# Kernel optimization log

Hardware: AMD Instinct MI355X
Metric: run time of the kernel (lower is better)

Reference implementation:

```python
import jax, jax.numpy as jnp
import numpy as np

B, V, T = 1, 1, 2
C = 128          # in_features
H = 4            # num_heads
NKV = 12288      # cells at cross zoom 5 (12*4**5)
S = NKV          # query groups == cross cells
NH = 9           # neighborhood size (cell + 8 ring)
NPQ = 16         # queries per group: 4**(7-5)
NQ = S * NPQ     # cells at zoom 7


def _ln(x, scale, bias, eps=1e-5):
    mu = jnp.mean(x, axis=-1, keepdims=True)
    var = jnp.mean(jnp.square(x - mu), axis=-1, keepdims=True)
    return (x - mu) * jax.lax.rsqrt(var + eps) * scale + bias


def setup_inputs() -> dict:
    key = jax.random.key(0)
    ks = jax.random.split(key, 12)
    w = lambda k, shp: jax.random.normal(k, shp, jnp.float32) * (1.0 / np.sqrt(shp[0]))
    return {
        "x_q":  jax.random.normal(ks[0], (B, V, T, NQ, C), jnp.float32),
        "x_kv": jax.random.normal(ks[1], (B, V, T, NKV, C), jnp.float32),
        "nh_idx":  jax.random.randint(ks[2], (S, NH), 0, NKV, jnp.int32),
        "nh_mask": jnp.ones((S, NH), jnp.bool_),
        "ln_q_s": jnp.ones((C,), jnp.float32), "ln_q_b": jnp.zeros((C,), jnp.float32),
        "Wq": w(ks[3], (C, C)), "bq": jnp.zeros((C,), jnp.float32),
        "ln_kv_s": jnp.ones((C,), jnp.float32), "ln_kv_b": jnp.zeros((C,), jnp.float32),
        "Wkv": w(ks[4], (C, 2 * C)), "bkv": jnp.zeros((2 * C,), jnp.float32),
        "Wa_q": w(ks[5], (C, C)),
        "W_out": w(ks[6], (C, C)), "b_out": jnp.zeros((C,), jnp.float32),
        "gamma": jnp.full((C,), 1e-6, jnp.float32),
        "ln_m_s": jnp.ones((C,), jnp.float32), "ln_m_b": jnp.zeros((C,), jnp.float32),
        "Wm": w(ks[7], (C, C)), "bm": jnp.zeros((C,), jnp.float32),
        "W1": w(ks[8], (C, C)), "b1": jnp.zeros((C,), jnp.float32),
        "W2": w(ks[9], (C, C)), "b2": jnp.zeros((C,), jnp.float32),
        "gamma_mlp": jnp.full((C,), 1e-6, jnp.float32),
    }


def reference(x_q, x_kv, nh_idx, nh_mask, ln_q_s, ln_q_b, Wq, bq,
              ln_kv_s, ln_kv_b, Wkv, bkv, Wa_q, W_out, b_out, gamma,
              ln_m_s, ln_m_b, Wm, bm, W1, b1, W2, b2, gamma_mlp):
    hd = C // H
    # q_layer: LN + Linear
    q = _ln(x_q, ln_q_s, ln_q_b) @ Wq + bq                      # [B,V,T,NQ,C]
    # kv_layer: LN + Linear to 2C (K|V)
    kv = _ln(x_kv, ln_kv_s, ln_kv_b) @ Wkv + bkv                # [B,V,T,NKV,2C]
    # grid neighborhood gather (get_nh)
    kv_nh = kv[:, :, :, nh_idx, :]                              # [B,V,T,S,NH,2C]
    k, vv = jnp.split(kv_nh, 2, axis=-1)                        # [B,V,T,S,NH,C] each
    # group queries per cross cell
    q = q.reshape(B, V, T, S, NPQ, C)
    # cross attention (q projected inside attention; k/v pre-projected)
    qh = (q @ Wa_q).reshape(B, V, T, S, NPQ, H, hd)
    kh = k.reshape(B, V, T, S, NH, H, hd)
    vh = vv.reshape(B, V, T, S, NH, H, hd)
    scores = jnp.einsum('bvtsqhd,bvtsnhd->bvtshqn', qh, kh) / np.sqrt(hd)
    bias = jnp.where(nh_mask, 0.0, -1e9).astype(scores.dtype)   # mask==False -> masked
    scores = scores + bias[None, None, None, :, None, None, :]
    attn = jax.nn.softmax(scores, axis=-1)
    out = jnp.einsum('bvtshqn,bvtsnhd->bvtsqhd', attn, vh).reshape(B, V, T, S, NPQ, C)
    out = out @ W_out + b_out
    x = x_q + gamma * out.reshape(B, V, T, NQ, C)
    # gated MLP residual
    h = _ln(x, ln_m_s, ln_m_b) @ Wm + bm
    m = jax.nn.gelu(h @ W1 + b1) @ W2 + b2
    x = x + gamma_mlp * m
    return x
```

## Files before the change

### kernel.cpp

```cpp
#include <hip/hip_runtime.h>
#include <hip/hip_bf16.h>

#define DEVINL __device__ __forceinline__

typedef __attribute__((ext_vector_type(8))) short bf16x8;
typedef __attribute__((ext_vector_type(4))) float f32x4;

static constexpr int SS = 12288;
static constexpr float QKS = 0.17677669529663687f;

DEVINL f32x4 f32x4_zero() { f32x4 z; z[0]=0.f; z[1]=0.f; z[2]=0.f; z[3]=0.f; return z; }
DEVINL f32x4 mfma16(bf16x8 a, bf16x8 b, f32x4 c) {
  return __builtin_amdgcn_mfma_f32_16x16x32_bf16(a, b, c, 0, 0, 0);
}
DEVINL unsigned short f2bf(float f) {
  __hip_bfloat16 h = __float2bfloat16(f);
  return __builtin_bit_cast(unsigned short, h);
}
DEVINL float bf2f(unsigned short u) {
  unsigned v = ((unsigned)u) << 16;
  return __builtin_bit_cast(float, v);
}
DEVINL unsigned cvt_pk_bf16(float lo_, float hi_) {
  unsigned r;
  asm volatile("v_cvt_pk_bf16_f32 %0, %1, %2" : "=v"(r) : "v"(lo_), "v"(hi_));
  return r;
}
DEVINL int swz(int r, int c) {
  return (r << 7) + ((((c >> 3) ^ (r & 7))) << 3) + (c & 7);
}
DEVINL void wave_sync() {
  asm volatile("s_waitcnt lgkmcnt(0)" ::: "memory");
  __builtin_amdgcn_sched_barrier(0);
}
DEVINL float gelu_f(float x) {
  float u = 0.7978845608028654f * (x + 0.044715f * x * x * x);
  float t = 1.0f - 2.0f / (__expf(2.0f * u) + 1.0f);
  return 0.5f * x * (1.0f + t);
}

DEVINL void stage8(const unsigned short* __restrict__ wf_all,
                   unsigned short* slot, int slice, int tid) {
  const unsigned short* src = wf_all + (size_t)slice * 4096;
  const int wv = tid >> 6, l = tid & 63;
#pragma unroll
  for (int r = 0; r < 2; ++r) {
    int off = (r * 4 + wv) * 512;
    __builtin_amdgcn_global_load_lds(
        (const __attribute__((address_space(1))) unsigned int*)(src + off + l * 8),
        (__attribute__((address_space(3))) unsigned int*)(slot + off), 16, 0, 0);
  }
}

__global__ void prep_weights(const float* __restrict__ w0, const float* __restrict__ w1,
                             const float* __restrict__ w2, const float* __restrict__ w3,
                             const float* __restrict__ w4, const float* __restrict__ w5,
                             unsigned short* __restrict__ wfrag) {
  int gid = blockIdx.x * 256 + threadIdx.x;
  int i  = gid & 7;
  int l  = (gid >> 3) & 63;
  int mt = (gid >> 9) & 7;
  int kt = (gid >> 12) & 3;
  int mat = gid >> 14;
  const float* W = (mat == 0) ? w0 : (mat == 1) ? w1 : (mat == 2) ? w2
                 : (mat == 3) ? w3 : (mat == 4) ? w4 : w5;
  int k = kt * 32 + (l >> 4) * 8 + i;
  int c = mt * 16 + (l & 15);
  float v = W[k * 128 + c];
  if (mat == 1) v *= QKS;
  wfrag[gid] = f2bf(v);
}

__global__ __launch_bounds__(256) void kv_proj(
    const float* __restrict__ xkv, const float* __restrict__ lns,
    const float* __restrict__ lnb, const float* __restrict__ Wkv,
    const float* __restrict__ bkv, unsigned short* __restrict__ kvout) {
  __shared__ float y[16][132];
  const int tid = threadIdx.x;
  const size_t rb = (size_t)blockIdx.x * 16;
  {
    int r = tid >> 4, p = tid & 15;
    const float* xr = xkv + (rb + r) * 128 + p * 8;
    float v[8];
    float sum = 0.f, sq = 0.f;
#pragma unroll
    for (int i = 0; i < 2; ++i) {
      float4 q4 = *(const float4*)(xr + i * 4);
      v[i*4+0]=q4.x; v[i*4+1]=q4.y; v[i*4+2]=q4.z; v[i*4+3]=q4.w;
      sum += q4.x + q4.y + q4.z + q4.w;
      sq  += q4.x*q4.x + q4.y*q4.y + q4.z*q4.z + q4.w*q4.w;
    }
    sum += __shfl_xor(sum, 1, 16); sum += __shfl_xor(sum, 2, 16);
    sum += __shfl_xor(sum, 4, 16); sum += __shfl_xor(sum, 8, 16);
    sq  += __shfl_xor(sq, 1, 16);  sq  += __shfl_xor(sq, 2, 16);
    sq  += __shfl_xor(sq, 4, 16);  sq  += __shfl_xor(sq, 8, 16);
    float mu = sum * (1.0f/128.f);
    float rs = rsqrtf(sq * (1.0f/128.f) - mu*mu + 1e-5f);
#pragma unroll
    for (int i = 0; i < 8; ++i) {
      int c = p * 8 + i;
      y[r][c] = (v[i] - mu) * rs * lns[c] + lnb[c];
    }
  }
  __syncthreads();
  const int c2 = tid;
  float acc[16];
#pragma unroll
  for (int r = 0; r < 16; ++r) acc[r] = 0.f;
  for (int c = 0; c < 128; c += 4) {
    float w0 = Wkv[(c+0)*256 + c2];
    float w1 = Wkv[(c+1)*256 + c2];
    float w2 = Wkv[(c+2)*256 + c2];
    float w3 = Wkv[(c+3)*256 + c2];
#pragma unroll
    for (int r = 0; r < 16; ++r) {
      float4 yv = *(const float4*)&y[r][c];
      acc[r] += yv.x*w0 + yv.y*w1 + yv.z*w2 + yv.w*w3;
    }
  }
  float bb = bkv[c2];
#pragma unroll
  for (int r = 0; r < 16; ++r)
    kvout[(rb + r) * 256 + c2] = f2bf(acc[r] + bb);
}

template <int MODE>
DEVINL void mmFlip(unsigned short* X, unsigned short (*Wb)[4096],
                   const unsigned short* __restrict__ wf_all, int j0,
                   const float* __restrict__ bias,
                   const float* __restrict__ xqw, const float* __restrict__ gamma,
                   unsigned* x2p, const float* __restrict__ gmlp,
                   float* __restrict__ outw, int tid) {
  const int l = tid & 63, lo = l & 15, g = l >> 4;
  f32x4 acc[8];
#pragma unroll
  for (int mt = 0; mt < 8; ++mt) acc[mt] = f32x4_zero();

#pragma unroll
  for (int kt = 0; kt < 4; ++kt) {
    const int j = j0 + kt;
    if (j + 1 < 24) stage8(wf_all, Wb[(j + 1) & 1], j + 1, tid);
    const unsigned short* W = Wb[j & 1];
    bf16x8 b = *(const bf16x8*)(X + swz(lo, kt * 32 + g * 8));
#pragma unroll
    for (int mt = 0; mt < 8; ++mt) {
      bf16x8 a = *(const bf16x8*)(W + (mt * 64 + l) * 8);
      acc[mt] = mfma16(a, b, acc[mt]);
    }
    __syncthreads();
  }

#pragma unroll
  for (int mt = 0; mt < 8; ++mt) {
    int c0 = mt * 16 + g * 4;
    float v0 = acc[mt][0], v1 = acc[mt][1], v2 = acc[mt][2], v3 = acc[mt][3];
    if (bias) {
      float4 b4 = *(const float4*)(bias + c0);
      v0 += b4.x; v1 += b4.y; v2 += b4.z; v3 += b4.w;
    }
    if (MODE == 1) { v0 = gelu_f(v0); v1 = gelu_f(v1); v2 = gelu_f(v2); v3 = gelu_f(v3); }
    if (MODE == 2) {
      float4 x4 = *(const float4*)(xqw + lo * 128 + c0);
      float4 g4 = *(const float4*)(gamma + c0);
      v0 = x4.x + g4.x * v0; v1 = x4.y + g4.y * v1;
      v2 = x4.z + g4.z * v2; v3 = x4.w + g4.w * v3;
      x2p[2 * mt]     = cvt_pk_bf16(v0, v1);
      x2p[2 * mt + 1] = cvt_pk_bf16(v2, v3);
    } else if (MODE == 3) {
      float4 p4 = *(const float4*)(gmlp + c0);
      unsigned xa = x2p[2 * mt], xb = x2p[2 * mt + 1];
      float4 o;
      o.x = bf2f((unsigned short)(xa & 0xffff))  + p4.x * v0;
      o.y = bf2f((unsigned short)(xa >> 16))     + p4.y * v1;
      o.z = bf2f((unsigned short)(xb & 0xffff))  + p4.z * v2;
      o.w = bf2f((unsigned short)(xb >> 16))     + p4.w * v3;
      *(float4*)(outw + lo * 128 + c0) = o;
    } else {
      uint2 w2;
      w2.x = cvt_pk_bf16(v0, v1);
      w2.y = cvt_pk_bf16(v2, v3);
      *(uint2*)(X + swz(lo, c0)) = w2;
    }
  }
}

__global__ __launch_bounds__(256, 3) void fused_main(
    const float* __restrict__ xq, const int* __restrict__ nh_idx,
    const unsigned char* __restrict__ nh_mask,
    const unsigned short* __restrict__ wfrag,
    const unsigned short* __restrict__ kvws,
    const float* __restrict__ ln_q_s, const float* __restrict__ ln_q_b,
    const float* __restrict__ bq, const float* __restrict__ b_out,
    const float* __restrict__ gamma, const float* __restrict__ ln_m_s,
    const float* __restrict__ ln_m_b, const float* __restrict__ bm,
    const float* __restrict__ b1, const float* __restrict__ b2,
    const float* __restrict__ gmlp, float* __restrict__ out) {
  __shared__ __align__(16) unsigned short Wb[2][4096];
  __shared__ __align__(16) unsigned short SU[4][3200];

  const int tid = threadIdx.x, l = tid & 63, wv = tid >> 6;
  const int lo = l & 15, g = l >> 4;
  const int nwg = gridDim.x;
  const int cpx = nwg >> 3;
  const int bid = (blockIdx.x & 7) * cpx + (blockIdx.x >> 3);
  const int su = bid * 4 + wv;
  const int t = su / SS, s = su - t * SS;
  const float* xqw = xq + (size_t)su * 2048;
  float* outw = out + (size_t)su * 2048;
  unsigned short* X = SU[wv];
  unsigned short* K = SU[wv] + 2048;

  stage8(wfrag, Wb[0], 0, tid);
  float sbias[4];
#pragma unroll
  for (int e = 0; e < 4; ++e) {
    int n = g * 4 + e;
    sbias[e] = (n < 9) ? (nh_mask[s * 9 + n] ? 0.0f : -1e9f) : -1e9f;
  }
  uint4 gr[5];
  {
#pragma unroll
    for (int i = 0; i < 5; ++i) {
      int idx = i * 64 + l;
      if (idx < 288) {
        int n = idx >> 5, ch = idx & 31;
        int jrow = nh_idx[s * 9 + n];
        gr[i] = *(const uint4*)(kvws + ((size_t)(t * SS + jrow)) * 256 + ch * 8);
      }
    }
#pragma unroll
    for (int i = 0; i < 5; ++i) {
      int idx = i * 64 + l;
      if (idx < 288 && (idx & 31) < 16) {
        int n = idx >> 5, ch = idx & 31;
        *(uint4*)(K + n * 128 + ((ch ^ (n & 7)) << 3)) = gr[i];
      }
    }
  }

  {
    float4 xv[8];
    float sum = 0.f, sq = 0.f;
#pragma unroll
    for (int mt = 0; mt < 8; ++mt) {
      xv[mt] = *(const float4*)(xqw + lo * 128 + mt * 16 + g * 4);
      sum += xv[mt].x + xv[mt].y + xv[mt].z + xv[mt].w;
      sq  += xv[mt].x*xv[mt].x + xv[mt].y*xv[mt].y + xv[mt].z*xv[mt].z + xv[mt].w*xv[mt].w;
    }
    sum += __shfl_xor(sum, 16); sum += __shfl_xor(sum, 32);
    sq  += __shfl_xor(sq, 16);  sq  += __shfl_xor(sq, 32);
    float mu = sum * (1.0f/128.f);
    float rs = rsqrtf(sq * (1.0f/128.f) - mu*mu + 1e-5f);
#pragma unroll
    for (int mt = 0; mt < 8; ++mt) {
      int c0 = mt * 16 + g * 4;
      float4 s4 = *(const float4*)(ln_q_s + c0);
      float4 b4 = *(const float4*)(ln_q_b + c0);
      uint2 w2;
      w2.x = cvt_pk_bf16((xv[mt].x - mu) * rs * s4.x + b4.x,
                         (xv[mt].y - mu) * rs * s4.y + b4.y);
      w2.y = cvt_pk_bf16((xv[mt].z - mu) * rs * s4.z + b4.z,
                         (xv[mt].w - mu) * rs * s4.w + b4.w);
      *(uint2*)(X + swz(lo, c0)) = w2;
    }
  }
  wave_sync();
  __syncthreads();

  unsigned x2p[16];

  mmFlip<0>(X, Wb, wfrag, 0, bq, nullptr, nullptr, nullptr, nullptr, nullptr, tid);
  wave_sync();
  mmFlip<0>(X, Wb, wfrag, 4, nullptr, nullptr, nullptr, nullptr, nullptr, nullptr, tid);
  wave_sync();

  {
    const int krow = (lo > 8) ? 8 : lo;
    f32x4 st[4];
    __builtin_amdgcn_s_setprio(1);
#pragma unroll
    for (int h = 0; h < 4; ++h) {
      bf16x8 ka = *(const bf16x8*)(K + swz(krow, h * 32 + g * 8));
      bf16x8 qb = *(const bf16x8*)(X + swz(lo,   h * 32 + g * 8));
      st[h] = mfma16(ka, qb, f32x4_zero());
    }
    __builtin_amdgcn_s_setprio(0);
    wave_sync();
#pragma unroll
    for (int i = 0; i < 5; ++i) {
      int idx = i * 64 + l;
      if (idx < 288 && (idx & 31) >= 16) {
        int n = idx >> 5, d0 = ((idx & 31) - 16) * 8;
        int nt = d0 >> 4;
        int base = nt * 256 + (n >> 1) * 32 + (d0 & 15) * 2 + (n & 1);
        const unsigned short* u = (const unsigned short*)&gr[i];
#pragma unroll
        for (int dd = 0; dd < 8; ++dd) X[base + dd * 2] = u[dd];
      }
    }
    bf16x8 pfrag[4];
#pragma unroll
    for (int h = 0; h < 4; ++h) {
      float p0 = st[h][0] + sbias[0], p1 = st[h][1] + sbias[1];
      float p2 = st[h][2] + sbias[2], p3 = st[h][3] + sbias[3];
      float m = fmaxf(fmaxf(p0, p1), fmaxf(p2, p3));
      m = fmaxf(m, __shfl_xor(m, 16)); m = fmaxf(m, __shfl_xor(m, 32));
      p0 = __expf(p0 - m); p1 = __expf(p1 - m);
      p2 = __expf(p2 - m); p3 = __expf(p3 - m);
      float ss = p0 + p1 + p2 + p3;
      ss += __shfl_xor(ss, 16); ss += __shfl_xor(ss, 32);
      float inv = 1.0f / ss;
      p0 *= inv; p1 *= inv; p2 *= inv; p3 *= inv;
      float b0 = __shfl_xor(p0, 16), b1 = __shfl_xor(p1, 16),
            b2_ = __shfl_xor(p2, 16), b3 = __shfl_xor(p3, 16);
      float c0_ = __shfl_xor(p0, 32), c1 = __shfl_xor(p1, 32),
            c2 = __shfl_xor(p2, 32), c3 = __shfl_xor(p3, 32);
      float d0_ = __shfl_xor(p0, 48), d1 = __shfl_xor(p1, 48),
            d2 = __shfl_xor(p2, 48), d3 = __shfl_xor(p3, 48);
      float L0 = (g == 0) ? p0 : (g == 1) ? d0_ : 0.f;
      float L1 = (g == 0) ? p1 : (g == 1) ? d1 : 0.f;
      float L2 = (g == 0) ? p2 : (g == 1) ? d2 : 0.f;
      float L3 = (g == 0) ? p3 : (g == 1) ? d3 : 0.f;
      float H0 = (g == 0) ? b0 : (g == 1) ? c0_ : 0.f;
      float H1 = (g == 0) ? b1 : (g == 1) ? c1 : 0.f;
      float H2 = (g == 0) ? b2_ : (g == 1) ? c2 : 0.f;
      float H3 = (g == 0) ? b3 : (g == 1) ? c3 : 0.f;
      uint4 pu;
      pu.x = cvt_pk_bf16(L0, L1); pu.y = cvt_pk_bf16(L2, L3);
      pu.z = cvt_pk_bf16(H0, H1); pu.w = cvt_pk_bf16(H2, H3);
      pfrag[h] = __builtin_bit_cast(bf16x8, pu);
    }
    wave_sync();
    f32x4 oacc[8];
    __builtin_amdgcn_s_setprio(1);
#pragma unroll
    for (int nt = 0; nt < 8; ++nt) {
      unsigned vw0 = 0, vw1 = 0, vw2 = 0, vw3 = 0;
      if (g < 2) {
        const unsigned short* vb = X + nt * 256 + g * 128 + lo * 2;
        vw0 = *(const unsigned*)(vb);
        vw1 = *(const unsigned*)(vb + 32);
        vw2 = *(const unsigned*)(vb + 64);
        vw3 = *(const unsigned*)(vb + 96);
      }
      uint4 vu; vu.x = vw0; vu.y = vw1; vu.z = vw2; vu.w = vw3;
      bf16x8 vfrag = __builtin_bit_cast(bf16x8, vu);
      oacc[nt] = mfma16(pfrag[nt >> 1], vfrag, f32x4_zero());
    }
    __builtin_amdgcn_s_setprio(0);
    wave_sync();
#pragma unroll
    for (int nt = 0; nt < 8; ++nt)
#pragma unroll
      for (int e = 0; e < 4; ++e)
        X[swz(g * 4 + e, nt * 16 + lo)] = (unsigned short)(cvt_pk_bf16(oacc[nt][e], 0.f) & 0xffff);
    wave_sync();
  }

  mmFlip<2>(X, Wb, wfrag, 8, b_out, xqw, gamma, x2p, nullptr, nullptr, tid);

  {
    float sum = 0.f, sq = 0.f;
#pragma unroll
    for (int mt = 0; mt < 8; ++mt) {
      unsigned xa = x2p[2*mt], xb = x2p[2*mt+1];
      float v0 = bf2f((unsigned short)(xa & 0xffff));
      float v1 = bf2f((unsigned short)(xa >> 16));
      float v2 = bf2f((unsigned short)(xb & 0xffff));
      float v3 = bf2f((unsigned short)(xb >> 16));
      sum += v0 + v1 + v2 + v3;
      sq  += v0*v0 + v1*v1 + v2*v2 + v3*v3;
    }
    sum += __shfl_xor(sum, 16); sum += __shfl_xor(sum, 32);
    sq  += __shfl_xor(sq, 16);  sq  += __shfl_xor(sq, 32);
    float mu = sum * (1.0f/128.f);
    float rs = rsqrtf(sq * (1.0f/128.f) - mu*mu + 1e-5f);
#pragma unroll
    for (int mt = 0; mt < 8; ++mt) {
      int c0 = mt * 16 + g * 4;
      unsigned xa = x2p[2*mt], xb = x2p[2*mt+1];
      float4 s4 = *(const float4*)(ln_m_s + c0);
      float4 b4 = *(const float4*)(ln_m_b + c0);
      uint2 w2;
      w2.x = cvt_pk_bf16((bf2f((unsigned short)(xa & 0xffff)) - mu) * rs * s4.x + b4.x,
                         (bf2f((unsigned short)(xa >> 16))    - mu) * rs * s4.y + b4.y);
      w2.y = cvt_pk_bf16((bf2f((unsigned short)(xb & 0xffff)) - mu) * rs * s4.z + b4.z,
                         (bf2f((unsigned short)(xb >> 16))    - mu) * rs * s4.w + b4.w);
      *(uint2*)(X + swz(lo, c0)) = w2;
    }
  }
  wave_sync();

  mmFlip<0>(X, Wb, wfrag, 12, bm, nullptr, nullptr, nullptr, nullptr, nullptr, tid);
  wave_sync();
  mmFlip<1>(X, Wb, wfrag, 16, b1, nullptr, nullptr, nullptr, nullptr, nullptr, tid);
  wave_sync();
  mmFlip<3>(X, Wb, wfrag, 20, b2, nullptr, nullptr, x2p, gmlp, outw, tid);
}

extern "C" void kernel_launch(void* const* d_in, const int* in_sizes, int n_in,
                              void* d_out, int out_size, void* d_ws, size_t ws_size,
                              hipStream_t stream) {
  const float* x_q     = (const float*)d_in[0];
  const float* x_kv    = (const float*)d_in[1];
  const int* nh_idx    = (const int*)d_in[2];
  const unsigned char* nh_mask = (const unsigned char*)d_in[3];
  const float* ln_q_s  = (const float*)d_in[4];
  const float* ln_q_b  = (const float*)d_in[5];
  const float* Wq      = (const float*)d_in[6];
  const float* bq      = (const float*)d_in[7];
  const float* ln_kv_s = (const float*)d_in[8];
  const float* ln_kv_b = (const float*)d_in[9];
  const float* Wkv     = (const float*)d_in[10];
  const float* bkv     = (const float*)d_in[11];
  const float* Wa_q    = (const float*)d_in[12];
  const float* W_out   = (const float*)d_in[13];
  const float* b_out   = (const float*)d_in[14];
  const float* gamma   = (const float*)d_in[15];
  const float* ln_m_s  = (const float*)d_in[16];
  const float* ln_m_b  = (const float*)d_in[17];
  const float* Wm      = (const float*)d_in[18];
  const float* bm      = (const float*)d_in[19];
  const float* W1      = (const float*)d_in[20];
  const float* b1      = (const float*)d_in[21];
  const float* W2      = (const float*)d_in[22];
  const float* b2      = (const float*)d_in[23];
  const float* gmlp    = (const float*)d_in[24];

  unsigned short* wfrag = (unsigned short*)d_ws;
  unsigned short* kvws  = wfrag + 6 * 16384;

  prep_weights<<<384, 256, 0, stream>>>(Wq, Wa_q, W_out, Wm, W1, W2, wfrag);
  kv_proj<<<1536, 256, 0, stream>>>(x_kv, ln_kv_s, ln_kv_b, Wkv, bkv, kvws);
  fused_main<<<6144, 256, 0, stream>>>(
      x_q, nh_idx, nh_mask, wfrag, kvws, ln_q_s, ln_q_b, bq, b_out, gamma,
      ln_m_s, ln_m_b, bm, b1, b2, gmlp, (float*)d_out);
}
```

Baseline: 348.9 us.

## Load weight fragments directly from global into registers, drop LDS staging and block barriers

Weight fragments for the six 128x128 matmuls were staged into a shared double buffer with global_load_lds, and a __syncthreads followed every k-step. Each wave now reads its MFMA A-fragments straight from global memory (L2-resident) into a register double buffer, which removes the block-wide barriers and 16 KB of LDS. Waves can then run independently and occupancy may rise. The cost is that every wave re-fetches all the weights instead of sharing them across the block, so L2 traffic goes up fourfold and register pressure grows with 16 bf16x8 buffers.

Result: slower. 392.0 us (+12.4%).

```diff
diff --git a/kernel.cpp b/kernel.cpp
--- a/kernel.cpp
+++ b/kernel.cpp
@@ -37,19 +37,6 @@
   float u = 0.7978845608028654f * (x + 0.044715f * x * x * x);
   float t = 1.0f - 2.0f / (__expf(2.0f * u) + 1.0f);
   return 0.5f * x * (1.0f + t);
-}
-
-DEVINL void stage8(const unsigned short* __restrict__ wf_all,
-                   unsigned short* slot, int slice, int tid) {
-  const unsigned short* src = wf_all + (size_t)slice * 4096;
-  const int wv = tid >> 6, l = tid & 63;
-#pragma unroll
-  for (int r = 0; r < 2; ++r) {
-    int off = (r * 4 + wv) * 512;
-    __builtin_amdgcn_global_load_lds(
-        (const __attribute__((address_space(1))) unsigned int*)(src + off + l * 8),
-        (__attribute__((address_space(3))) unsigned int*)(slot + off), 16, 0, 0);
-  }
 }
 
 __global__ void prep_weights(const float* __restrict__ w0, const float* __restrict__ w1,
@@ -125,29 +112,32 @@
 }
 
 template <int MODE>
-DEVINL void mmFlip(unsigned short* X, unsigned short (*Wb)[4096],
-                   const unsigned short* __restrict__ wf_all, int j0,
-                   const float* __restrict__ bias,
-                   const float* __restrict__ xqw, const float* __restrict__ gamma,
-                   unsigned* x2p, const float* __restrict__ gmlp,
-                   float* __restrict__ outw, int tid) {
-  const int l = tid & 63, lo = l & 15, g = l >> 4;
+DEVINL void mmReg(unsigned short* X, const unsigned short* __restrict__ wmat,
+                  const float* __restrict__ bias,
+                  const float* __restrict__ xqw, const float* __restrict__ gamma,
+                  unsigned* x2p, const float* __restrict__ gmlp,
+                  float* __restrict__ outw, int lo, int g, int l) {
   f32x4 acc[8];
 #pragma unroll
   for (int mt = 0; mt < 8; ++mt) acc[mt] = f32x4_zero();
 
+  const unsigned short* wl = wmat + l * 8;
+  bf16x8 w[2][8];
+#pragma unroll
+  for (int mt = 0; mt < 8; ++mt)
+    w[0][mt] = *(const bf16x8*)(wl + mt * 512);
+
 #pragma unroll
   for (int kt = 0; kt < 4; ++kt) {
-    const int j = j0 + kt;
-    if (j + 1 < 24) stage8(wf_all, Wb[(j + 1) & 1], j + 1, tid);
-    const unsigned short* W = Wb[j & 1];
+    if (kt < 3) {
+#pragma unroll
+      for (int mt = 0; mt < 8; ++mt)
+        w[(kt + 1) & 1][mt] = *(const bf16x8*)(wl + (kt + 1) * 4096 + mt * 512);
+    }
     bf16x8 b = *(const bf16x8*)(X + swz(lo, kt * 32 + g * 8));
 #pragma unroll
-    for (int mt = 0; mt < 8; ++mt) {
-      bf16x8 a = *(const bf16x8*)(W + (mt * 64 + l) * 8);
-      acc[mt] = mfma16(a, b, acc[mt]);
-    }
-    __syncthreads();
+    for (int mt = 0; mt < 8; ++mt)
+      acc[mt] = mfma16(w[kt & 1][mt], b, acc[mt]);
   }
 
 #pragma unroll
@@ -195,7 +185,6 @@
     const float* __restrict__ ln_m_b, const float* __restrict__ bm,
     const float* __restrict__ b1, const float* __restrict__ b2,
     const float* __restrict__ gmlp, float* __restrict__ out) {
-  __shared__ __align__(16) unsigned short Wb[2][4096];
   __shared__ __align__(16) unsigned short SU[4][3200];
 
   const int tid = threadIdx.x, l = tid & 63, wv = tid >> 6;
@@ -210,7 +199,6 @@
   unsigned short* X = SU[wv];
   unsigned short* K = SU[wv] + 2048;
 
-  stage8(wfrag, Wb[0], 0, tid);
   float sbias[4];
 #pragma unroll
   for (int e = 0; e < 4; ++e) {
@@ -265,13 +253,12 @@
     }
   }
   wave_sync();
-  __syncthreads();
 
   unsigned x2p[16];
 
-  mmFlip<0>(X, Wb, wfrag, 0, bq, nullptr, nullptr, nullptr, nullptr, nullptr, tid);
-  wave_sync();
-  mmFlip<0>(X, Wb, wfrag, 4, nullptr, nullptr, nullptr, nullptr, nullptr, nullptr, tid);
+  mmReg<0>(X, wfrag + 0 * 16384, bq, nullptr, nullptr, nullptr, nullptr, nullptr, lo, g, l);
+  wave_sync();
+  mmReg<0>(X, wfrag + 1 * 16384, nullptr, nullptr, nullptr, nullptr, nullptr, nullptr, lo, g, l);
   wave_sync();
 
   {
@@ -357,7 +344,7 @@
     wave_sync();
   }
 
-  mmFlip<2>(X, Wb, wfrag, 8, b_out, xqw, gamma, x2p, nullptr, nullptr, tid);
+  mmReg<2>(X, wfrag + 2 * 16384, b_out, xqw, gamma, x2p, nullptr, nullptr, lo, g, l);
 
   {
     float sum = 0.f, sq = 0.f;
@@ -391,11 +378,11 @@
   }
   wave_sync();
 
-  mmFlip<0>(X, Wb, wfrag, 12, bm, nullptr, nullptr, nullptr, nullptr, nullptr, tid);
-  wave_sync();
-  mmFlip<1>(X, Wb, wfrag, 16, b1, nullptr, nullptr, nullptr, nullptr, nullptr, tid);
-  wave_sync();
-  mmFlip<3>(X, Wb, wfrag, 20, b2, nullptr, nullptr, x2p, gmlp, outw, tid);
+  mmReg<0>(X, wfrag + 3 * 16384, bm, nullptr, nullptr, nullptr, nullptr, nullptr, lo, g, l);
+  wave_sync();
+  mmReg<1>(X, wfrag + 4 * 16384, b1, nullptr, nullptr, nullptr, nullptr, nullptr, lo, g, l);
+  wave_sync();
+  mmReg<3>(X, wfrag + 5 * 16384, b2, nullptr, nullptr, x2p, gmlp, outw, lo, g, l);
 }
 
 extern "C" void kernel_launch(void* const* d_in, const int* in_sizes, int n_in,
```
